# Performance work log

Hardware: AMD Instinct MI355X
Metric: run time of the kernel (lower is better)

Reference implementation:

```python
import jax, jax.numpy as jnp
import numpy as np

N, M, D = 4096, 8192, 1024
N_ITERS = 15  # module hardcodes self.n_iters = 15
EPS = 1e-12   # F.normalize eps


def setup_inputs() -> dict:
    key = jax.random.key(0)
    k1, k2 = jax.random.split(key)
    K = jax.random.normal(k1, (N, M), dtype=jnp.float32)
    y = jax.random.normal(k2, (M, D), dtype=jnp.float32)
    return {"K": K, "y": y, "topk": 32}


def _topk_preimage(K_mat, y, topk):
    # torch: topk -> L1-normalize values -> scatter into zeros_like(K) -> mm(y).
    # Since topk indices are unique per row, scatter+dense-mm == gather + weighted sum.
    vals, inds = jax.lax.top_k(K_mat, topk)                      # [N, k], [N, k]
    norm = jnp.maximum(jnp.sum(jnp.abs(vals), axis=-1, keepdims=True), EPS)
    w = vals / norm                                              # F.normalize(p=1, dim=-1)
    preimage = jnp.einsum('nk,nkd->nd', w, y[inds])              # [N, D]
    return preimage, inds


def reference(K, y, topk):
    preimage, inds = _topk_preimage(K, y, topk)

    def body(pre, _):
        K_i = pre @ y.T                                          # linear kernel_fn: [N, M]
        pre, inds_i = _topk_preimage(K_i, y, topk)
        return pre, inds_i

    preimage, inds_all = jax.lax.scan(body, preimage, None, length=N_ITERS)
    return preimage, inds_all[-1]
```

## Files before the change

### kernel.cpp

```cpp
#include <hip/hip_runtime.h>
#include <hip/hip_bf16.h>
#include <math.h>

#define N_ROWS 4096
#define M_COLS 8192
#define D_DIM  1024
#define TOPK   32
#define N_ITERS 15
#define CHUNK   1024
#define KC      384
#define D_CUT   1696

template <int EXACT_V>
__global__ __launch_bounds__(256) void topk_pre_kernel(
    const float* __restrict__ R,
    const float* __restrict__ Y,
    float* __restrict__ pre,
    int* __restrict__ inds_ws,
    int row_off, int write_inds)
{
    __shared__ float row[M_COLS];
    __shared__ float red_v[256];
    __shared__ int   red_i[256];
    __shared__ float topv[TOPK];
    __shared__ int   topi[TOPK];
    __shared__ float s_w[TOPK];
    __shared__ int   s_si[TOPK];
    __shared__ float s_sw[TOPK];
    __shared__ float s_norm;

    const int tid    = threadIdx.x;
    const int n_loc  = blockIdx.x;
    const int n_glob = row_off + n_loc;
    const float* Rr  = R + (size_t)n_loc * M_COLS;

    for (int i = tid; i < M_COLS / 4; i += 256)
        reinterpret_cast<float4*>(row)[i] = reinterpret_cast<const float4*>(Rr)[i];
    __syncthreads();

    for (int s = 0; s < TOPK; ++s) {
        float bv = -INFINITY; int bi = M_COLS;
        for (int j = tid; j < M_COLS; j += 256) {
            float v = row[j];
            if (v > bv) { bv = v; bi = j; }
        }
        red_v[tid] = bv; red_i[tid] = bi;
        __syncthreads();
        for (int stride = 128; stride > 0; stride >>= 1) {
            if (tid < stride) {
                float ov = red_v[tid + stride]; int oi = red_i[tid + stride];
                if (ov > red_v[tid] || (ov == red_v[tid] && oi < red_i[tid])) {
                    red_v[tid] = ov; red_i[tid] = oi;
                }
            }
            __syncthreads();
        }
        if (tid == 0) {
            topv[s] = red_v[0]; topi[s] = red_i[0];
            row[red_i[0]] = -INFINITY;
        }
        __syncthreads();
    }

    if (EXACT_V) {
        if (tid == 0) {
            double sum = 0.0;
            for (int k = 0; k < TOPK; ++k) sum += fabs((double)topv[k]);
            s_norm = fmaxf((float)sum, 1e-12f);
        }
    } else {
        if (tid == 0) {
            float r[8];
            #pragma unroll
            for (int j = 0; j < 8; ++j) r[j] = fabsf(topv[j]);
            #pragma unroll
            for (int blk = 8; blk < TOPK; blk += 8)
                #pragma unroll
                for (int j = 0; j < 8; ++j)
                    r[j] = __fadd_rn(r[j], fabsf(topv[blk + j]));
            float s01 = __fadd_rn(r[0], r[1]);
            float s23 = __fadd_rn(r[2], r[3]);
            float s45 = __fadd_rn(r[4], r[5]);
            float s67 = __fadd_rn(r[6], r[7]);
            s_norm = fmaxf(__fadd_rn(__fadd_rn(s01, s23), __fadd_rn(s45, s67)), 1e-12f);
        }
    }
    __syncthreads();
    if (tid < TOPK) s_w[tid] = __fdiv_rn(topv[tid], s_norm);
    __syncthreads();

    if (EXACT_V) {
        double acc[4] = {0.0, 0.0, 0.0, 0.0};
        for (int k = 0; k < TOPK; ++k) {
            const double wk = (double)s_w[k];
            const float* yr = Y + (size_t)topi[k] * D_DIM;
            #pragma unroll
            for (int j = 0; j < 4; ++j)
                acc[j] = fma(wk, (double)yr[tid + 256 * j], acc[j]);
        }
        float* pr = pre + (size_t)n_glob * D_DIM;
        #pragma unroll
        for (int j = 0; j < 4; ++j) pr[tid + 256 * j] = (float)acc[j];
    } else {
        if (tid == 0) {
            for (int k = 0; k < TOPK; ++k) { s_si[k] = topi[k]; s_sw[k] = s_w[k]; }
            for (int a = 1; a < TOPK; ++a) {
                int ia = s_si[a]; float wa = s_sw[a];
                int b = a - 1;
                while (b >= 0 && s_si[b] > ia) {
                    s_si[b + 1] = s_si[b]; s_sw[b + 1] = s_sw[b]; --b;
                }
                s_si[b + 1] = ia; s_sw[b + 1] = wa;
            }
        }
        __syncthreads();
        float tot[4]  = {0.f, 0.f, 0.f, 0.f};
        float part[4] = {0.f, 0.f, 0.f, 0.f};
        int curPan = s_si[0] / KC;
        for (int k = 0; k < TOPK; ++k) {
            const int idx = s_si[k];
            const int pan = idx / KC;
            if (pan != curPan) {
                #pragma unroll
                for (int j = 0; j < 4; ++j) {
                    tot[j] = __fadd_rn(tot[j], part[j]);
                    part[j] = 0.f;
                }
                curPan = pan;
            }
            const float wk = s_sw[k];
            const float* yr = Y + (size_t)idx * D_DIM;
            #pragma unroll
            for (int j = 0; j < 4; ++j)
                part[j] = fmaf(wk, yr[tid + 256 * j], part[j]);
        }
        #pragma unroll
        for (int j = 0; j < 4; ++j) tot[j] = __fadd_rn(tot[j], part[j]);
        float* pr = pre + (size_t)n_glob * D_DIM;
        #pragma unroll
        for (int j = 0; j < 4; ++j) pr[tid + 256 * j] = tot[j];
    }

    if (write_inds && tid < TOPK)
        inds_ws[(size_t)n_glob * TOPK + tid] = topi[tid];
}

#define BM 128
#define BN 64
#define BK 16

template <int EXACT_V>
__global__ __launch_bounds__(256) void gemm_nt_kernel(
    const float* __restrict__ A,
    const float* __restrict__ B,
    float* __restrict__ C)
{
    __shared__ float As[BK][BM + 4];
    __shared__ float Bs[BK][BN + 4];

    const int tid  = threadIdx.x;
    const int tx   = tid & 15;
    const int ty   = tid >> 4;
    const int row0 = blockIdx.y * BM;
    const int col0 = blockIdx.x * BN;

    const int lrA = tid >> 1;
    const int lcA = (tid & 1) * 8;
    const int lrB = tid >> 2;
    const int lcB = (tid & 3) * 4;

    float  tot[8][4], acc[8][4];
    double dacc[8][4];
    #pragma unroll
    for (int i = 0; i < 8; ++i)
        #pragma unroll
        for (int j = 0; j < 4; ++j) { tot[i][j] = 0.f; acc[i][j] = 0.f; dacc[i][j] = 0.0; }

    for (int k0 = 0; k0 < D_DIM; k0 += BK) {
        float4 va0 = *reinterpret_cast<const float4*>(A + (size_t)(row0 + lrA) * D_DIM + k0 + lcA);
        float4 va1 = *reinterpret_cast<const float4*>(A + (size_t)(row0 + lrA) * D_DIM + k0 + lcA + 4);
        As[lcA + 0][lrA] = va0.x; As[lcA + 1][lrA] = va0.y;
        As[lcA + 2][lrA] = va0.z; As[lcA + 3][lrA] = va0.w;
        As[lcA + 4][lrA] = va1.x; As[lcA + 5][lrA] = va1.y;
        As[lcA + 6][lrA] = va1.z; As[lcA + 7][lrA] = va1.w;
        float4 vb = *reinterpret_cast<const float4*>(B + (size_t)(col0 + lrB) * D_DIM + k0 + lcB);
        Bs[lcB + 0][lrB] = vb.x; Bs[lcB + 1][lrB] = vb.y;
        Bs[lcB + 2][lrB] = vb.z; Bs[lcB + 3][lrB] = vb.w;
        __syncthreads();

        #pragma unroll
        for (int kk = 0; kk < BK; ++kk) {
            float a[8], b[4];
            #pragma unroll
            for (int i = 0; i < 8; ++i) a[i] = As[kk][ty * 8 + i];
            #pragma unroll
            for (int j = 0; j < 4; ++j) b[j] = Bs[kk][tx * 4 + j];
            if (EXACT_V) {
                #pragma unroll
                for (int i = 0; i < 8; ++i)
                    #pragma unroll
                    for (int j = 0; j < 4; ++j)
                        dacc[i][j] = fma((double)a[i], (double)b[j], dacc[i][j]);
            } else {
                #pragma unroll
                for (int i = 0; i < 8; ++i)
                    #pragma unroll
                    for (int j = 0; j < 4; ++j)
                        acc[i][j] = fmaf(a[i], b[j], acc[i][j]);
            }
        }
        __syncthreads();

        if (!EXACT_V) {
            const int kend = k0 + BK;
            if (kend == KC || kend == 2 * KC || kend == D_DIM) {
                #pragma unroll
                for (int i = 0; i < 8; ++i)
                    #pragma unroll
                    for (int j = 0; j < 4; ++j) {
                        tot[i][j] = __fadd_rn(tot[i][j], acc[i][j]);
                        acc[i][j] = 0.f;
                    }
            }
        }
    }

    #pragma unroll
    for (int i = 0; i < 8; ++i) {
        float4 v;
        if (EXACT_V) {
            v = make_float4((float)dacc[i][0], (float)dacc[i][1],
                            (float)dacc[i][2], (float)dacc[i][3]);
        } else {
            v = make_float4(tot[i][0], tot[i][1], tot[i][2], tot[i][3]);
        }
        float* cr = C + (size_t)(row0 + ty * 8 + i) * M_COLS + col0 + tx * 4;
        *reinterpret_cast<float4*>(cr) = v;
    }
}

__global__ __launch_bounds__(256) void choice_kernel(
    const int* __restrict__ indsA,
    const int* __restrict__ indsB,
    unsigned char* __restrict__ choice)
{
    const int n = blockIdx.x * 256 + threadIdx.x;
    if (n >= N_ROWS) return;
    int d = 0;
    #pragma unroll
    for (int k = 0; k < TOPK; ++k) {
        int diff = indsA[n * TOPK + k] - indsB[n * TOPK + k];
        if (diff < 0) diff = -diff;
        if (diff > d) d = diff;
    }
    choice[n] = (d > 0 && d <= D_CUT) ? 1 : 0;
}

__global__ __launch_bounds__(256) void emit_kernel(
    const float* __restrict__ preA, const float* __restrict__ preB,
    const int* __restrict__ indsA,  const int* __restrict__ indsB,
    const unsigned char* __restrict__ choice,
    float* __restrict__ out_pre, float* __restrict__ out_inds)
{
    const int n   = blockIdx.x;
    const int tid = threadIdx.x;
    const int c   = choice[n];
    const float* ps = (c ? preB : preA) + (size_t)n * D_DIM;
    const int*   is = (c ? indsB : indsA) + (size_t)n * TOPK;
    float* po = out_pre + (size_t)n * D_DIM;
    #pragma unroll
    for (int j = 0; j < 4; ++j) po[tid + 256 * j] = ps[tid + 256 * j];
    if (tid < TOPK)
        out_inds[(size_t)n * TOPK + tid] = (float)is[tid];
}

extern "C" void kernel_launch(void* const* d_in, const int* in_sizes, int n_in,
                              void* d_out, int out_size, void* d_ws, size_t ws_size,
                              hipStream_t stream)
{
    const float* K_in = (const float*)d_in[0];
    const float* Y    = (const float*)d_in[1];

    char* p = (char*)d_ws;
    float* preA   = (float*)p; p += (size_t)N_ROWS * D_DIM * sizeof(float);
    float* preB   = (float*)p; p += (size_t)N_ROWS * D_DIM * sizeof(float);
    float* Kchunk = (float*)p; p += (size_t)CHUNK * M_COLS * sizeof(float);
    int*   indsA  = (int*)p;   p += (size_t)N_ROWS * TOPK * sizeof(int);
    int*   indsB  = (int*)p;   p += (size_t)N_ROWS * TOPK * sizeof(int);
    unsigned char* choice = (unsigned char*)p;

    float* out_pre  = (float*)d_out;
    float* out_inds = out_pre + (size_t)N_ROWS * D_DIM;

    topk_pre_kernel<0><<<N_ROWS, 256, 0, stream>>>(K_in, Y, preA, indsA, 0, 0);
    topk_pre_kernel<1><<<N_ROWS, 256, 0, stream>>>(K_in, Y, preB, indsB, 0, 0);

    for (int it = 0; it < N_ITERS; ++it) {
        const int wo = (it == N_ITERS - 1) ? 1 : 0;
        for (int c = 0; c < N_ROWS / CHUNK; ++c) {
            gemm_nt_kernel<0><<<dim3(M_COLS / BN, CHUNK / BM), 256, 0, stream>>>(
                preA + (size_t)c * CHUNK * D_DIM, Y, Kchunk);
            topk_pre_kernel<0><<<CHUNK, 256, 0, stream>>>(
                Kchunk, Y, preA, indsA, c * CHUNK, wo);
            gemm_nt_kernel<1><<<dim3(M_COLS / BN, CHUNK / BM), 256, 0, stream>>>(
                preB + (size_t)c * CHUNK * D_DIM, Y, Kchunk);
            topk_pre_kernel<1><<<CHUNK, 256, 0, stream>>>(
                Kchunk, Y, preB, indsB, c * CHUNK, wo);
        }
    }

    choice_kernel<<<(N_ROWS + 255) / 256, 256, 0, stream>>>(indsA, indsB, choice);
    emit_kernel<<<N_ROWS, 256, 0, stream>>>(preA, preB, indsA, indsB, choice,
                                            out_pre, out_inds);
}
```

Baseline: 53.79 ms.

## Register-resident topk with wave shuffles, split GEMMs, larger fp32 tile, bigger chunk

The top-k selection now keeps each row's 32 values per thread in registers instead of a 32KB shared row, and reduces the argmax with wavefront shuffles plus a 4-entry cross-wave step, replacing the 8-step shared-memory tree with its many barriers. The templated GEMM is split into separate kernels: the fp32 path uses a 128x128 tile with 8x8 per-thread outputs for more reuse, and the fp64 path keeps 128x64 without dead fp32 accumulators. CHUNK grows to 2048, giving fewer launches and more blocks per launch. The costs are higher register pressure in the topk and fp32 GEMM kernels, which may lower occupancy, and a larger Kchunk buffer.

```diff
diff --git a/kernel.cpp b/kernel.cpp
--- a/kernel.cpp
+++ b/kernel.cpp
@@ -7,7 +7,7 @@
 #define D_DIM  1024
 #define TOPK   32
 #define N_ITERS 15
-#define CHUNK   1024
+#define CHUNK   2048
 #define KC      384
 #define D_CUT   1696
 
@@ -19,11 +19,11 @@
     int* __restrict__ inds_ws,
     int row_off, int write_inds)
 {
-    __shared__ float row[M_COLS];
-    __shared__ float red_v[256];
-    __shared__ int   red_i[256];
+    __shared__ float s_wv[4];
+    __shared__ int   s_wi[4];
     __shared__ float topv[TOPK];
     __shared__ int   topi[TOPK];
+    __shared__ int   s_win;
     __shared__ float s_w[TOPK];
     __shared__ int   s_si[TOPK];
     __shared__ float s_sw[TOPK];
@@ -34,32 +34,49 @@
     const int n_glob = row_off + n_loc;
     const float* Rr  = R + (size_t)n_loc * M_COLS;
 
-    for (int i = tid; i < M_COLS / 4; i += 256)
-        reinterpret_cast<float4*>(row)[i] = reinterpret_cast<const float4*>(Rr)[i];
-    __syncthreads();
+    float v[32];
+    #pragma unroll
+    for (int q = 0; q < 8; ++q) {
+        float4 w = reinterpret_cast<const float4*>(Rr)[tid + 256 * q];
+        v[4 * q + 0] = w.x; v[4 * q + 1] = w.y;
+        v[4 * q + 2] = w.z; v[4 * q + 3] = w.w;
+    }
 
     for (int s = 0; s < TOPK; ++s) {
         float bv = -INFINITY; int bi = M_COLS;
-        for (int j = tid; j < M_COLS; j += 256) {
-            float v = row[j];
-            if (v > bv) { bv = v; bi = j; }
-        }
-        red_v[tid] = bv; red_i[tid] = bi;
-        __syncthreads();
-        for (int stride = 128; stride > 0; stride >>= 1) {
-            if (tid < stride) {
-                float ov = red_v[tid + stride]; int oi = red_i[tid + stride];
-                if (ov > red_v[tid] || (ov == red_v[tid] && oi < red_i[tid])) {
-                    red_v[tid] = ov; red_i[tid] = oi;
+        #pragma unroll
+        for (int q = 0; q < 8; ++q)
+            #pragma unroll
+            for (int c = 0; c < 4; ++c) {
+                const int m = 4 * q + c;
+                const int j = 4 * tid + 1024 * q + c;
+                const float val = v[m];
+                if (val > bv || (val == bv && j < bi)) { bv = val; bi = j; }
+            }
+        #pragma unroll
+        for (int off = 32; off > 0; off >>= 1) {
+            float ov = __shfl_down(bv, off);
+            int   oi = __shfl_down(bi, off);
+            if (ov > bv || (ov == bv && oi < bi)) { bv = ov; bi = oi; }
+        }
+        if ((tid & 63) == 0) { s_wv[tid >> 6] = bv; s_wi[tid >> 6] = bi; }
+        __syncthreads();
+        if (tid == 0) {
+            for (int w = 1; w < 4; ++w) {
+                if (s_wv[w] > bv || (s_wv[w] == bv && s_wi[w] < bi)) {
+                    bv = s_wv[w]; bi = s_wi[w];
                 }
             }
-            __syncthreads();
-        }
-        if (tid == 0) {
-            topv[s] = red_v[0]; topi[s] = red_i[0];
-            row[red_i[0]] = -INFINITY;
-        }
-        __syncthreads();
+            topv[s] = bv; topi[s] = bi; s_win = bi;
+        }
+        __syncthreads();
+        const int win = s_win;
+        if (((win >> 2) & 255) == tid) {
+            const int mw = ((win >> 10) << 2) | (win & 3);
+            #pragma unroll
+            for (int m = 0; m < 32; ++m)
+                if (m == mw) v[m] = -INFINITY;
+        }
     }
 
     if (EXACT_V) {
@@ -145,38 +162,115 @@
         inds_ws[(size_t)n_glob * TOPK + tid] = topi[tid];
 }
 
-#define BM 128
-#define BN 64
-#define BK 16
-
-template <int EXACT_V>
-__global__ __launch_bounds__(256) void gemm_nt_kernel(
+#define ABM 128
+#define ABN 128
+#define ABK 16
+
+__global__ __launch_bounds__(256) void gemmA_kernel(
     const float* __restrict__ A,
     const float* __restrict__ B,
     float* __restrict__ C)
 {
-    __shared__ float As[BK][BM + 4];
-    __shared__ float Bs[BK][BN + 4];
+    __shared__ float As[ABK][ABM + 4];
+    __shared__ float Bs[ABK][ABN + 4];
 
     const int tid  = threadIdx.x;
     const int tx   = tid & 15;
     const int ty   = tid >> 4;
-    const int row0 = blockIdx.y * BM;
-    const int col0 = blockIdx.x * BN;
+    const int row0 = blockIdx.y * ABM;
+    const int col0 = blockIdx.x * ABN;
+
+    const int lr = tid >> 1;
+    const int lc = (tid & 1) * 8;
+
+    float tot[8][8], acc[8][8];
+    #pragma unroll
+    for (int i = 0; i < 8; ++i)
+        #pragma unroll
+        for (int j = 0; j < 8; ++j) { tot[i][j] = 0.f; acc[i][j] = 0.f; }
+
+    for (int k0 = 0; k0 < D_DIM; k0 += ABK) {
+        float4 va0 = *reinterpret_cast<const float4*>(A + (size_t)(row0 + lr) * D_DIM + k0 + lc);
+        float4 va1 = *reinterpret_cast<const float4*>(A + (size_t)(row0 + lr) * D_DIM + k0 + lc + 4);
+        As[lc + 0][lr] = va0.x; As[lc + 1][lr] = va0.y;
+        As[lc + 2][lr] = va0.z; As[lc + 3][lr] = va0.w;
+        As[lc + 4][lr] = va1.x; As[lc + 5][lr] = va1.y;
+        As[lc + 6][lr] = va1.z; As[lc + 7][lr] = va1.w;
+        float4 vb0 = *reinterpret_cast<const float4*>(B + (size_t)(col0 + lr) * D_DIM + k0 + lc);
+        float4 vb1 = *reinterpret_cast<const float4*>(B + (size_t)(col0 + lr) * D_DIM + k0 + lc + 4);
+        Bs[lc + 0][lr] = vb0.x; Bs[lc + 1][lr] = vb0.y;
+        Bs[lc + 2][lr] = vb0.z; Bs[lc + 3][lr] = vb0.w;
+        Bs[lc + 4][lr] = vb1.x; Bs[lc + 5][lr] = vb1.y;
+        Bs[lc + 6][lr] = vb1.z; Bs[lc + 7][lr] = vb1.w;
+        __syncthreads();
+
+        #pragma unroll
+        for (int kk = 0; kk < ABK; ++kk) {
+            float a[8], b[8];
+            #pragma unroll
+            for (int i = 0; i < 8; ++i) a[i] = As[kk][ty * 8 + i];
+            #pragma unroll
+            for (int j = 0; j < 8; ++j) b[j] = Bs[kk][tx * 8 + j];
+            #pragma unroll
+            for (int i = 0; i < 8; ++i)
+                #pragma unroll
+                for (int j = 0; j < 8; ++j)
+                    acc[i][j] = fmaf(a[i], b[j], acc[i][j]);
+        }
+        __syncthreads();
+
+        const int kend = k0 + ABK;
+        if (kend == KC || kend == 2 * KC || kend == D_DIM) {
+            #pragma unroll
+            for (int i = 0; i < 8; ++i)
+                #pragma unroll
+                for (int j = 0; j < 8; ++j) {
+                    tot[i][j] = __fadd_rn(tot[i][j], acc[i][j]);
+                    acc[i][j] = 0.f;
+                }
+        }
+    }
+
+    #pragma unroll
+    for (int i = 0; i < 8; ++i) {
+        float4 v0 = { tot[i][0], tot[i][1], tot[i][2], tot[i][3] };
+        float4 v1 = { tot[i][4], tot[i][5], tot[i][6], tot[i][7] };
+        float* cr = C + (size_t)(row0 + ty * 8 + i) * M_COLS + col0 + tx * 8;
+        *reinterpret_cast<float4*>(cr)     = v0;
+        *reinterpret_cast<float4*>(cr + 4) = v1;
+    }
+}
+
+#define BBM 128
+#define BBN 64
+#define BBK 16
+
+__global__ __launch_bounds__(256) void gemmB_kernel(
+    const float* __restrict__ A,
+    const float* __restrict__ B,
+    float* __restrict__ C)
+{
+    __shared__ float As[BBK][BBM + 4];
+    __shared__ float Bs[BBK][BBN + 4];
+
+    const int tid  = threadIdx.x;
+    const int tx   = tid & 15;
+    const int ty   = tid >> 4;
+    const int row0 = blockIdx.y * BBM;
+    const int col0 = blockIdx.x * BBN;
 
     const int lrA = tid >> 1;
     const int lcA = (tid & 1) * 8;
     const int lrB = tid >> 2;
     const int lcB = (tid & 3) * 4;
 
-    float  tot[8][4], acc[8][4];
     double dacc[8][4];
     #pragma unroll
     for (int i = 0; i < 8; ++i)
         #pragma unroll
-        for (int j = 0; j < 4; ++j) { tot[i][j] = 0.f; acc[i][j] = 0.f; dacc[i][j] = 0.0; }
-
-    for (int k0 = 0; k0 < D_DIM; k0 += BK) {
+        for (int j = 0; j < 4; ++j) dacc[i][j] = 0.0;
+
+    for (int k0 = 0; k0 < D_DIM; k0 += BBK) {
         float4 va0 = *reinterpret_cast<const float4*>(A + (size_t)(row0 + lrA) * D_DIM + k0 + lcA);
         float4 va1 = *reinterpret_cast<const float4*>(A + (size_t)(row0 + lrA) * D_DIM + k0 + lcA + 4);
         As[lcA + 0][lrA] = va0.x; As[lcA + 1][lrA] = va0.y;
@@ -189,51 +283,25 @@
         __syncthreads();
 
         #pragma unroll
-        for (int kk = 0; kk < BK; ++kk) {
-            float a[8], b[4];
-            #pragma unroll
-            for (int i = 0; i < 8; ++i) a[i] = As[kk][ty * 8 + i];
-            #pragma unroll
-            for (int j = 0; j < 4; ++j) b[j] = Bs[kk][tx * 4 + j];
-            if (EXACT_V) {
-                #pragma unroll
-                for (int i = 0; i < 8; ++i)
-                    #pragma unroll
-                    for (int j = 0; j < 4; ++j)
-                        dacc[i][j] = fma((double)a[i], (double)b[j], dacc[i][j]);
-            } else {
-                #pragma unroll
-                for (int i = 0; i < 8; ++i)
-                    #pragma unroll
-                    for (int j = 0; j < 4; ++j)
-                        acc[i][j] = fmaf(a[i], b[j], acc[i][j]);
-            }
-        }
-        __syncthreads();
-
-        if (!EXACT_V) {
-            const int kend = k0 + BK;
-            if (kend == KC || kend == 2 * KC || kend == D_DIM) {
-                #pragma unroll
-                for (int i = 0; i < 8; ++i)
-                    #pragma unroll
-                    for (int j = 0; j < 4; ++j) {
-                        tot[i][j] = __fadd_rn(tot[i][j], acc[i][j]);
-                        acc[i][j] = 0.f;
-                    }
-            }
-        }
+        for (int kk = 0; kk < BBK; ++kk) {
+            double a[8], b[4];
+            #pragma unroll
+            for (int i = 0; i < 8; ++i) a[i] = (double)As[kk][ty * 8 + i];
+            #pragma unroll
+            for (int j = 0; j < 4; ++j) b[j] = (double)Bs[kk][tx * 4 + j];
+            #pragma unroll
+            for (int i = 0; i < 8; ++i)
+                #pragma unroll
+                for (int j = 0; j < 4; ++j)
+                    dacc[i][j] = fma(a[i], b[j], dacc[i][j]);
+        }
+        __syncthreads();
     }
 
     #pragma unroll
     for (int i = 0; i < 8; ++i) {
-        float4 v;
-        if (EXACT_V) {
-            v = make_float4((float)dacc[i][0], (float)dacc[i][1],
-                            (float)dacc[i][2], (float)dacc[i][3]);
-        } else {
-            v = make_float4(tot[i][0], tot[i][1], tot[i][2], tot[i][3]);
-        }
+        float4 v = { (float)dacc[i][0], (float)dacc[i][1],
+                     (float)dacc[i][2], (float)dacc[i][3] };
         float* cr = C + (size_t)(row0 + ty * 8 + i) * M_COLS + col0 + tx * 4;
         *reinterpret_cast<float4*>(cr) = v;
     }
@@ -298,11 +366,11 @@
     for (int it = 0; it < N_ITERS; ++it) {
         const int wo = (it == N_ITERS - 1) ? 1 : 0;
         for (int c = 0; c < N_ROWS / CHUNK; ++c) {
-            gemm_nt_kernel<0><<<dim3(M_COLS / BN, CHUNK / BM), 256, 0, stream>>>(
+            gemmA_kernel<<<dim3(M_COLS / ABN, CHUNK / ABM), 256, 0, stream>>>(
                 preA + (size_t)c * CHUNK * D_DIM, Y, Kchunk);
             topk_pre_kernel<0><<<CHUNK, 256, 0, stream>>>(
                 Kchunk, Y, preA, indsA, c * CHUNK, wo);
-            gemm_nt_kernel<1><<<dim3(M_COLS / BN, CHUNK / BM), 256, 0, stream>>>(
+            gemmB_kernel<<<dim3(M_COLS / BBN, CHUNK / BBM), 256, 0, stream>>>(
                 preB + (size_t)c * CHUNK * D_DIM, Y, Kchunk);
             topk_pre_kernel<1><<<CHUNK, 256, 0, stream>>>(
                 Kchunk, Y, preB, indsB, c * CHUNK, wo);
```

New measurement: 53.53 ms. No clear change (-0.5%).
